# Optimization experiments

Measured on AMD Instinct MI355X. Metric: run time of the kernel, lower is better.

The kernel has to match this reference:

```python
import jax, jax.numpy as jnp
import numpy as np

B, C, S, H, W, J = 4, 256, 256, 128, 128, 8
BN_EPS = 1e-5


def _conv3x3(x, w, b):
    # x: [B,S,H,W], w: [C,S,3,3] (OIHW), SAME padding, stride 1
    y = jax.lax.conv_general_dilated(x, w, window_strides=(1, 1), padding='SAME',
                                     dimension_numbers=('NCHW', 'OIHW', 'NCHW'))
    return y + b[None, :, None, None]


def setup_inputs() -> dict:
    key = jax.random.key(0)
    ks = jax.random.split(key, 12)
    fp = jax.random.normal(ks[0], (B, C, H, W), jnp.float32)
    labels = jax.random.randint(ks[1], (B, H, W), 0, J)
    sg = jax.nn.one_hot(labels, J, axis=1, dtype=jnp.float32)  # [B,J,H,W], disjoint masks
    style_codes = jax.random.normal(ks[2], (B, J + 1, S), jnp.float32)
    mask_codes = jax.random.randint(ks[3], (B, J), 0, 2)  # 0 or 1
    bn_gamma = 1.0 + 0.1 * jax.random.normal(ks[4], (C,), jnp.float32)
    bn_beta = 0.1 * jax.random.normal(ks[5], (C,), jnp.float32)
    W_mu = 0.05 * jax.random.normal(ks[6], (J, S, S), jnp.float32)
    b_mu = 0.05 * jax.random.normal(ks[7], (J, S), jnp.float32)
    W_gamma = 0.05 * jax.random.normal(ks[8], (C, S, 3, 3), jnp.float32)
    b_gamma = 0.05 * jax.random.normal(ks[9], (C,), jnp.float32)
    W_beta = 0.05 * jax.random.normal(ks[10], (C, S, 3, 3), jnp.float32)
    b_beta = 0.05 * jax.random.normal(ks[11], (C,), jnp.float32)
    return {"fp": fp, "sg": sg, "style_codes": style_codes, "mask_codes": mask_codes,
            "bn_gamma": bn_gamma, "bn_beta": bn_beta, "W_mu": W_mu, "b_mu": b_mu,
            "W_gamma": W_gamma, "b_gamma": b_gamma, "W_beta": W_beta, "b_beta": b_beta}


def reference(fp, sg, style_codes, mask_codes, bn_gamma, bn_beta,
              W_mu, b_mu, W_gamma, b_gamma, W_beta, b_beta):
    # BatchNorm2d (training mode, biased variance, affine)
    mean = jnp.mean(fp, axis=(0, 2, 3))
    var = jnp.mean(jnp.square(fp - mean[None, :, None, None]), axis=(0, 2, 3))
    nf = (fp - mean[None, :, None, None]) * jax.lax.rsqrt(var + BN_EPS)[None, :, None, None]
    nf = nf * bn_gamma[None, :, None, None] + bn_beta[None, :, None, None]

    # per-(batch,class) style code selection: j if mask_codes==1 else J (shared code)
    sel = jnp.where(mask_codes == 1, jnp.arange(J, dtype=mask_codes.dtype)[None, :], J)  # [B,J]
    codes = jnp.take_along_axis(style_codes, sel[:, :, None], axis=1)  # [B,J,S]

    # per-class FC + ReLU (torch Linear: y = x @ W.T + b)
    mu = jax.nn.relu(jnp.einsum('bjs,jos->bjo', codes, W_mu) + b_mu[None])  # [B,J,S]

    # scatter per-region style into spatial map (masks are disjoint one-hot)
    middle = jnp.einsum('bjhw,bjs->bshw', sg, mu)  # [B,S,H,W]

    gamma_avg = _conv3x3(middle, W_gamma, b_gamma)
    beta_avg = _conv3x3(middle, W_beta, b_beta)
    return nf * (1.0 + gamma_avg) + beta_avg
```

## Files before the change

### kernel.cpp

```cpp
#include <hip/hip_runtime.h>

#define Bb 4
#define Cc 256
#define Ss 256
#define Hh 128
#define Ww 128
#define Jj 8
#define HWp 16384
#define BN_EPS 1e-5f

#define WS_PS   0
#define WS_PQ   4096
#define WS_MU   10240
#define WS_LAB  43008
#define WS_WTG  108544
#define WS_WTB  2467840
#define WS_VT   4827136

#define VROW 160
#define ZOFF (81 * VROW)
#define SLICE (2 * ZOFF)
#define VBUF_B 26112

__global__ void k_prep(const float* __restrict__ fp, const float* __restrict__ sg,
                       const float* __restrict__ style, const int* __restrict__ mask,
                       const float* __restrict__ Wmu, const float* __restrict__ bmu,
                       const float* __restrict__ Wg, const float* __restrict__ Wb,
                       float* __restrict__ ws_f, unsigned char* __restrict__ labout,
                       float* __restrict__ muout,
                       float* __restrict__ wtg, float* __restrict__ wtb) {
    __shared__ float smem[1056];
    const int t = threadIdx.x;
    const int blk = blockIdx.x;
    if (blk < 1024) {
        const int c = blk >> 2, b = blk & 3;
        const float4* s4 = (const float4*)(fp + (size_t)(b * Cc + c) * HWp);
        float sum = 0.f, sq = 0.f;
        #pragma unroll
        for (int k = 0; k < 16; ++k) {
            float4 v = s4[t + k * 256];
            sum += v.x + v.y + v.z + v.w;
            sq  += v.x * v.x + v.y * v.y + v.z * v.z + v.w * v.w;
        }
        float* ls = smem;
        float* lq = smem + 256;
        ls[t] = sum; lq[t] = sq;
        __syncthreads();
        for (int off = 128; off > 0; off >>= 1) {
            if (t < off) { ls[t] += ls[t + off]; lq[t] += lq[t + off]; }
            __syncthreads();
        }
        if (t == 0) { ws_f[blk] = ls[0]; ws_f[1024 + blk] = lq[0]; }
    } else if (blk < 1280) {
        const int i = (blk - 1024) * 256 + t;
        const int b = i >> 14, p = i & (HWp - 1);
        const float* base = sg + (size_t)b * Jj * HWp + p;
        int l = 0;
        #pragma unroll
        for (int j = 0; j < Jj; ++j)
            if (base[(size_t)j * HWp] > 0.5f) l = j;
        labout[i] = (unsigned char)l;
    } else if (blk < 1312) {
        const int lb = blk - 1280;
        const int b = lb >> 3, j = lb & 7;
        const int sel = (mask[b * Jj + j] == 1) ? j : Jj;
        float* code = smem;
        code[t] = style[(size_t)(b * (Jj + 1) + sel) * Ss + t];
        __syncthreads();
        const float4* wrow = (const float4*)(Wmu + (size_t)(j * Ss + t) * Ss);
        const float4* c4 = (const float4*)code;
        float acc = bmu[j * Ss + t];
        #pragma unroll 8
        for (int s4i = 0; s4i < Ss / 4; ++s4i) {
            float4 w = wrow[s4i]; float4 cv = c4[s4i];
            acc += w.x * cv.x + w.y * cv.y + w.z * cv.z + w.w * cv.w;
        }
        muout[(size_t)lb * Ss + t] = fmaxf(acc, 0.f);
    } else {
        const int local = blk - 1312;
        const int z = local / 576;
        const int rem = local % 576;
        const int k0 = (rem % 72) * 32;
        const int r0 = (rem / 72) * 32;
        const float* in = z ? Wb : Wg;
        float* outp = z ? wtb : wtg;
        float (*tile)[33] = (float(*)[33])smem;
        const int tx = t & 31, ty = t >> 5;
        #pragma unroll
        for (int i2 = 0; i2 < 4; ++i2)
            tile[ty + 8 * i2][tx] = in[(size_t)(r0 + ty + 8 * i2) * 2304 + k0 + tx];
        __syncthreads();
        #pragma unroll
        for (int i2 = 0; i2 < 4; ++i2)
            outp[(size_t)(k0 + ty + 8 * i2) * 256 + r0 + tx] = tile[tx][ty + 8 * i2];
    }
}

__global__ void k_build(const float* __restrict__ bn_g, const float* __restrict__ bn_b,
                        const float* __restrict__ bgam, const float* __restrict__ bbet,
                        const float* __restrict__ wtg, const float* __restrict__ wtb,
                        const float* __restrict__ mu, float* __restrict__ ws_f,
                        float* __restrict__ vt) {
    const int t = threadIdx.x;
    if (blockIdx.x == 0) {
        float s = 0.f, q = 0.f;
        #pragma unroll
        for (int b = 0; b < 4; ++b) { s += ws_f[t * 4 + b]; q += ws_f[1024 + t * 4 + b]; }
        float mean = s * (1.f / 65536.f);
        float var  = q * (1.f / 65536.f) - mean * mean;
        float sc = bn_g[t] * rsqrtf(var + BN_EPS);
        float sh = bn_b[t] - mean * sc;
        ((float4*)ws_f)[t] = make_float4(sc, sh, 1.f + bgam[t], bbet[t]);
        return;
    }
    const int lb = blockIdx.x - 1;
    const int z = lb / 36;
    const int rem = lb % 36;
    const int tap = rem % 9, b = rem / 9;
    const float* Wt = z ? wtb : wtg;
    __shared__ __align__(16) float ml[Jj * Ss];
    for (int idx = t; idx < Jj * Ss; idx += 256)
        ml[idx] = mu[(size_t)b * Jj * Ss + (size_t)(idx & 7) * Ss + (idx >> 3)];
    __syncthreads();
    float ag[8] = {0,0,0,0,0,0,0,0};
    const float* wp = Wt + (size_t)tap * 256 + t;
    #pragma unroll 8
    for (int s = 0; s < Ss; ++s) {
        float wv = wp[(size_t)s * 2304];
        float4 m0 = *(const float4*)&ml[s * 8];
        float4 m1 = *(const float4*)&ml[s * 8 + 4];
        ag[0] += wv * m0.x; ag[1] += wv * m0.y;
        ag[2] += wv * m0.z; ag[3] += wv * m0.w;
        ag[4] += wv * m1.x; ag[5] += wv * m1.y;
        ag[6] += wv * m1.z; ag[7] += wv * m1.w;
    }
    const int cc = t >> 5, cl = t & 31;
    float* Vrow = vt + ((size_t)((cc * 4 + b) * 2 + z) * 81 + tap * 9) * 40 + cl;
    #pragma unroll
    for (int j = 0; j < 8; ++j) Vrow[j * 40] = ag[j];
    Vrow[8 * 40] = 0.f;
}

__global__ void __launch_bounds__(256, 4) k_main(
    const float* __restrict__ fp, const unsigned char* __restrict__ lab,
    const char* __restrict__ vt, const float4* __restrict__ T,
    float* __restrict__ out) {
    const int h0 = blockIdx.x * 4, cc = blockIdx.y, b = blockIdx.z;
    __shared__ __align__(16) char vbuf[VBUF_B];
    __shared__ int labs[6][132];
    __shared__ float4 Tl[32];
    const int t = threadIdx.x;
    const int lane = t & 63;
    const int wid = __builtin_amdgcn_readfirstlane(t >> 6);

    {
        const char* slice = vt + (size_t)(cc * 4 + b) * SLICE;
        for (int r = wid; r < 102; r += 4) {
            __builtin_amdgcn_global_load_lds(
                (const __attribute__((address_space(1))) void*)(slice + r * 256 + lane * 4),
                (__attribute__((address_space(3))) void*)(vbuf + r * 256), 4, 0, 0);
        }
    }
    if (t < 32) Tl[t] = T[cc * 32 + t];
    for (int idx = t; idx < 6 * 132; idx += 256) {
        const int r = idx / 132, col = idx % 132 - 1;
        const int hh = h0 - 1 + r;
        int v = 8;
        if (hh >= 0 && hh < Hh && col >= 0 && col < Ww)
            v = lab[((size_t)b << 14) + (hh << 7) + col];
        labs[r][idx % 132] = v;
    }
    __syncthreads();

    const int w = t & 127;
    const int cs = t >> 7;
    const int cbase = cc * 32 + cs * 16;

    for (int hh = 0; hh < 4; ++hh) {
        int vb0[9];
        #pragma unroll
        for (int tap = 0; tap < 9; ++tap) {
            const int j = labs[hh + tap / 3][w + tap % 3];
            vb0[tap] = (tap * 9 + j) * VROW + cs * 64;
        }
        const size_t io = ((size_t)(b * Cc + cbase) << 14) + ((h0 + hh) << 7) + w;
        const float* fpp = fp + io;
        float* outp = out + io;
        #pragma unroll
        for (int cb = 0; cb < 4; ++cb) {
            float4 ga = make_float4(0.f, 0.f, 0.f, 0.f);
            float4 ea = make_float4(0.f, 0.f, 0.f, 0.f);
            #pragma unroll
            for (int tap = 0; tap < 9; ++tap) {
                const float4 vg = *(const float4*)(vbuf + vb0[tap] + cb * 16);
                const float4 ve = *(const float4*)(vbuf + ZOFF + vb0[tap] + cb * 16);
                ga.x += vg.x; ga.y += vg.y; ga.z += vg.z; ga.w += vg.w;
                ea.x += ve.x; ea.y += ve.y; ea.z += ve.z; ea.w += ve.w;
            }
            #define APPLY(CI, GV, EV)                                              \
            {                                                                      \
                const int c = cb * 4 + CI;                                         \
                const float4 tv = Tl[cs * 16 + c];                                 \
                const float f = __builtin_nontemporal_load(fpp + (size_t)c * HWp); \
                const float nf = fmaf(f, tv.x, tv.y);                              \
                __builtin_nontemporal_store(fmaf(nf, tv.z + (GV), tv.w + (EV)),    \
                                            outp + (size_t)c * HWp);               \
            }
            APPLY(0, ga.x, ea.x)
            APPLY(1, ga.y, ea.y)
            APPLY(2, ga.z, ea.z)
            APPLY(3, ga.w, ea.w)
            #undef APPLY
        }
    }
}

extern "C" void kernel_launch(void* const* d_in, const int* in_sizes, int n_in,
                              void* d_out, int out_size, void* d_ws, size_t ws_size,
                              hipStream_t stream) {
    const float* fp      = (const float*)d_in[0];
    const float* sg      = (const float*)d_in[1];
    const float* style   = (const float*)d_in[2];
    const int*   mask    = (const int*)d_in[3];
    const float* bn_g    = (const float*)d_in[4];
    const float* bn_b    = (const float*)d_in[5];
    const float* W_mu    = (const float*)d_in[6];
    const float* b_mu    = (const float*)d_in[7];
    const float* W_gam   = (const float*)d_in[8];
    const float* b_gam   = (const float*)d_in[9];
    const float* W_bet   = (const float*)d_in[10];
    const float* b_bet   = (const float*)d_in[11];
    float* out = (float*)d_out;

    char* ws = (char*)d_ws;
    float*         ws_f  = (float*)ws;
    unsigned char* labp  = (unsigned char*)(ws + WS_LAB);
    float*         mup   = (float*)(ws + WS_MU);
    float*         wtg   = (float*)(ws + WS_WTG);
    float*         wtb   = (float*)(ws + WS_WTB);
    float*         vtp   = (float*)(ws + WS_VT);

    k_prep<<<2464, 256, 0, stream>>>(fp, sg, style, mask, W_mu, b_mu, W_gam, W_bet,
                                     ws_f, labp, mup, wtg, wtb);
    k_build<<<73, 256, 0, stream>>>(bn_g, bn_b, b_gam, b_bet, wtg, wtb, mup, ws_f, vtp);
    k_main<<<dim3(32, 8, 4), 256, 0, stream>>>(fp, labp, (const char*)vtp,
                                               (const float4*)ws_f, out);
}
```

Baseline: 71.57 us.

## Halve channels per main block, shrink LDS table, split build over class halves

The main kernel now covers 16 channels per block instead of 32, which halves its shared-memory table and doubles the grid. It raises the occupancy hint to 8 blocks per CU and stages the table with 16-byte global-to-LDS loads. The build kernel splits its work over two class halves to match the new per-slice layout and to launch more blocks. The trade-off is that label-tile loads and setup are repeated across twice as many blocks.

```diff
diff --git a/kernel.cpp b/kernel.cpp
--- a/kernel.cpp
+++ b/kernel.cpp
@@ -17,10 +17,10 @@
 #define WS_WTB  2467840
 #define WS_VT   4827136
 
-#define VROW 160
-#define ZOFF (81 * VROW)
-#define SLICE (2 * ZOFF)
-#define VBUF_B 26112
+#define VROW 80
+#define ZOFF 6480
+#define SLICE_B 13312
+#define SLICE_F 3328
 
 __global__ void k_prep(const float* __restrict__ fp, const float* __restrict__ sg,
                        const float* __restrict__ style, const int* __restrict__ mask,
@@ -114,54 +114,54 @@
         return;
     }
     const int lb = blockIdx.x - 1;
-    const int z = lb / 36;
-    const int rem = lb % 36;
-    const int tap = rem % 9, b = rem / 9;
+    const int z = lb / 72;
+    const int rem = lb % 72;
+    const int jh = rem / 36;
+    const int r2 = rem % 36;
+    const int tap = r2 % 9, b = r2 / 9;
     const float* Wt = z ? wtb : wtg;
-    __shared__ __align__(16) float ml[Jj * Ss];
-    for (int idx = t; idx < Jj * Ss; idx += 256)
-        ml[idx] = mu[(size_t)b * Jj * Ss + (size_t)(idx & 7) * Ss + (idx >> 3)];
+    __shared__ __align__(16) float ml[4 * Ss];
+    for (int idx = t; idx < 4 * Ss; idx += 256)
+        ml[idx] = mu[(size_t)b * Jj * Ss + (size_t)(jh * 4 + (idx & 3)) * Ss + (idx >> 2)];
     __syncthreads();
-    float ag[8] = {0,0,0,0,0,0,0,0};
+    float ag[4] = {0, 0, 0, 0};
     const float* wp = Wt + (size_t)tap * 256 + t;
     #pragma unroll 8
     for (int s = 0; s < Ss; ++s) {
         float wv = wp[(size_t)s * 2304];
-        float4 m0 = *(const float4*)&ml[s * 8];
-        float4 m1 = *(const float4*)&ml[s * 8 + 4];
-        ag[0] += wv * m0.x; ag[1] += wv * m0.y;
-        ag[2] += wv * m0.z; ag[3] += wv * m0.w;
-        ag[4] += wv * m1.x; ag[5] += wv * m1.y;
-        ag[6] += wv * m1.z; ag[7] += wv * m1.w;
-    }
-    const int cc = t >> 5, cl = t & 31;
-    float* Vrow = vt + ((size_t)((cc * 4 + b) * 2 + z) * 81 + tap * 9) * 40 + cl;
+        float4 m = *(const float4*)&ml[s * 4];
+        ag[0] += wv * m.x; ag[1] += wv * m.y;
+        ag[2] += wv * m.z; ag[3] += wv * m.w;
+    }
+    const int cc = t >> 4, cl = t & 15;
+    float* Vrow = vt + (size_t)(cc * 4 + b) * SLICE_F + z * 1620
+                + (tap * 9 + jh * 4) * 20 + cl;
     #pragma unroll
-    for (int j = 0; j < 8; ++j) Vrow[j * 40] = ag[j];
-    Vrow[8 * 40] = 0.f;
-}
-
-__global__ void __launch_bounds__(256, 4) k_main(
+    for (int jj = 0; jj < 4; ++jj) Vrow[jj * 20] = ag[jj];
+    if (jh == 1) Vrow[4 * 20] = 0.f;
+}
+
+__global__ void __launch_bounds__(256, 8) k_main(
     const float* __restrict__ fp, const unsigned char* __restrict__ lab,
     const char* __restrict__ vt, const float4* __restrict__ T,
     float* __restrict__ out) {
     const int h0 = blockIdx.x * 4, cc = blockIdx.y, b = blockIdx.z;
-    __shared__ __align__(16) char vbuf[VBUF_B];
+    __shared__ __align__(16) char vbuf[SLICE_B];
     __shared__ int labs[6][132];
-    __shared__ float4 Tl[32];
+    __shared__ float4 Tl[16];
     const int t = threadIdx.x;
     const int lane = t & 63;
     const int wid = __builtin_amdgcn_readfirstlane(t >> 6);
 
     {
-        const char* slice = vt + (size_t)(cc * 4 + b) * SLICE;
-        for (int r = wid; r < 102; r += 4) {
+        const char* slice = vt + (size_t)(cc * 4 + b) * SLICE_B;
+        for (int r = wid; r < 13; r += 4) {
             __builtin_amdgcn_global_load_lds(
-                (const __attribute__((address_space(1))) void*)(slice + r * 256 + lane * 4),
-                (__attribute__((address_space(3))) void*)(vbuf + r * 256), 4, 0, 0);
-        }
-    }
-    if (t < 32) Tl[t] = T[cc * 32 + t];
+                (const __attribute__((address_space(1))) void*)(slice + r * 1024 + lane * 16),
+                (__attribute__((address_space(3))) void*)(vbuf + r * 1024), 16, 0, 0);
+        }
+    }
+    if (t < 16) Tl[t] = T[cc * 16 + t];
     for (int idx = t; idx < 6 * 132; idx += 256) {
         const int r = idx / 132, col = idx % 132 - 1;
         const int hh = h0 - 1 + r;
@@ -174,20 +174,20 @@
 
     const int w = t & 127;
     const int cs = t >> 7;
-    const int cbase = cc * 32 + cs * 16;
+    const int cbase = cc * 16 + cs * 8;
 
     for (int hh = 0; hh < 4; ++hh) {
         int vb0[9];
         #pragma unroll
         for (int tap = 0; tap < 9; ++tap) {
             const int j = labs[hh + tap / 3][w + tap % 3];
-            vb0[tap] = (tap * 9 + j) * VROW + cs * 64;
+            vb0[tap] = (tap * 9 + j) * VROW + cs * 32;
         }
         const size_t io = ((size_t)(b * Cc + cbase) << 14) + ((h0 + hh) << 7) + w;
         const float* fpp = fp + io;
         float* outp = out + io;
         #pragma unroll
-        for (int cb = 0; cb < 4; ++cb) {
+        for (int cb = 0; cb < 2; ++cb) {
             float4 ga = make_float4(0.f, 0.f, 0.f, 0.f);
             float4 ea = make_float4(0.f, 0.f, 0.f, 0.f);
             #pragma unroll
@@ -200,7 +200,7 @@
             #define APPLY(CI, GV, EV)                                              \
             {                                                                      \
                 const int c = cb * 4 + CI;                                         \
-                const float4 tv = Tl[cs * 16 + c];                                 \
+                const float4 tv = Tl[cs * 8 + c];                                  \
                 const float f = __builtin_nontemporal_load(fpp + (size_t)c * HWp); \
                 const float nf = fmaf(f, tv.x, tv.y);                              \
                 __builtin_nontemporal_store(fmaf(nf, tv.z + (GV), tv.w + (EV)),    \
@@ -242,7 +242,7 @@
 
     k_prep<<<2464, 256, 0, stream>>>(fp, sg, style, mask, W_mu, b_mu, W_gam, W_bet,
                                      ws_f, labp, mup, wtg, wtb);
-    k_build<<<73, 256, 0, stream>>>(bn_g, bn_b, b_gam, b_bet, wtg, wtb, mup, ws_f, vtp);
-    k_main<<<dim3(32, 8, 4), 256, 0, stream>>>(fp, labp, (const char*)vtp,
-                                               (const float4*)ws_f, out);
-}
+    k_build<<<145, 256, 0, stream>>>(bn_g, bn_b, b_gam, b_bet, wtg, wtb, mup, ws_f, vtp);
+    k_main<<<dim3(32, 16, 4), 256, 0, stream>>>(fp, labp, (const char*)vtp,
+                                                (const float4*)ws_f, out);
+}
```

New measurement: 75.16 us. 5.0% more time.

## Interleave gamma/beta V table rows, halve rows per block, batch LDS loads

Applied to the files above, without the earlier changes.

The precomputed per-(tap,label) gamma and beta contributions are now stored interleaved in one 272-byte row instead of two separate planes. This shrinks each slice so it can be staged into LDS with 16-byte global_load_lds transfers. Each k_main block now handles 2 output rows instead of 4, so the grid doubles and launch bounds allow 8 blocks per CU, aiming at more occupancy and better latency hiding. The 9-tap reductions are split into grouped LDS loads with sched barriers and tree-shaped sums, trading more VGPRs and more repeated slice loads per output for higher memory-level parallelism.

```diff
diff --git a/kernel.cpp b/kernel.cpp
--- a/kernel.cpp
+++ b/kernel.cpp
@@ -17,10 +17,9 @@
 #define WS_WTB  2467840
 #define WS_VT   4827136
 
-#define VROW 160
-#define ZOFF (81 * VROW)
-#define SLICE (2 * ZOFF)
-#define VBUF_B 26112
+#define VROW 272
+#define SLICE_B 22528
+#define SLICE_F 5632
 
 __global__ void k_prep(const float* __restrict__ fp, const float* __restrict__ sg,
                        const float* __restrict__ style, const int* __restrict__ mask,
@@ -135,34 +134,34 @@
         ag[6] += wv * m1.z; ag[7] += wv * m1.w;
     }
     const int cc = t >> 5, cl = t & 31;
-    float* Vrow = vt + ((size_t)((cc * 4 + b) * 2 + z) * 81 + tap * 9) * 40 + cl;
+    float* base = vt + (size_t)(cc * 4 + b) * SLICE_F + z * 32 + cl;
     #pragma unroll
-    for (int j = 0; j < 8; ++j) Vrow[j * 40] = ag[j];
-    Vrow[8 * 40] = 0.f;
-}
-
-__global__ void __launch_bounds__(256, 4) k_main(
+    for (int j = 0; j < 8; ++j) base[(tap * 9 + j) * 68] = ag[j];
+    base[(tap * 9 + 8) * 68] = 0.f;
+}
+
+__global__ void __launch_bounds__(256, 8) k_main(
     const float* __restrict__ fp, const unsigned char* __restrict__ lab,
     const char* __restrict__ vt, const float4* __restrict__ T,
     float* __restrict__ out) {
-    const int h0 = blockIdx.x * 4, cc = blockIdx.y, b = blockIdx.z;
-    __shared__ __align__(16) char vbuf[VBUF_B];
-    __shared__ int labs[6][132];
+    const int h0 = blockIdx.x * 2, cc = blockIdx.y, b = blockIdx.z;
+    __shared__ __align__(16) char vbuf[SLICE_B];
+    __shared__ int labs[4][132];
     __shared__ float4 Tl[32];
     const int t = threadIdx.x;
     const int lane = t & 63;
     const int wid = __builtin_amdgcn_readfirstlane(t >> 6);
 
     {
-        const char* slice = vt + (size_t)(cc * 4 + b) * SLICE;
-        for (int r = wid; r < 102; r += 4) {
+        const char* slice = vt + (size_t)(cc * 4 + b) * SLICE_B;
+        for (int r = wid; r < 22; r += 4) {
             __builtin_amdgcn_global_load_lds(
-                (const __attribute__((address_space(1))) void*)(slice + r * 256 + lane * 4),
-                (__attribute__((address_space(3))) void*)(vbuf + r * 256), 4, 0, 0);
+                (const __attribute__((address_space(1))) void*)(slice + r * 1024 + lane * 16),
+                (__attribute__((address_space(3))) void*)(vbuf + r * 1024), 16, 0, 0);
         }
     }
     if (t < 32) Tl[t] = T[cc * 32 + t];
-    for (int idx = t; idx < 6 * 132; idx += 256) {
+    for (int idx = t; idx < 4 * 132; idx += 256) {
         const int r = idx / 132, col = idx % 132 - 1;
         const int hh = h0 - 1 + r;
         int v = 8;
@@ -176,7 +175,7 @@
     const int cs = t >> 7;
     const int cbase = cc * 32 + cs * 16;
 
-    for (int hh = 0; hh < 4; ++hh) {
+    for (int hh = 0; hh < 2; ++hh) {
         int vb0[9];
         #pragma unroll
         for (int tap = 0; tap < 9; ++tap) {
@@ -188,15 +187,34 @@
         float* outp = out + io;
         #pragma unroll
         for (int cb = 0; cb < 4; ++cb) {
-            float4 ga = make_float4(0.f, 0.f, 0.f, 0.f);
-            float4 ea = make_float4(0.f, 0.f, 0.f, 0.f);
+            float4 vg[9];
             #pragma unroll
-            for (int tap = 0; tap < 9; ++tap) {
-                const float4 vg = *(const float4*)(vbuf + vb0[tap] + cb * 16);
-                const float4 ve = *(const float4*)(vbuf + ZOFF + vb0[tap] + cb * 16);
-                ga.x += vg.x; ga.y += vg.y; ga.z += vg.z; ga.w += vg.w;
-                ea.x += ve.x; ea.y += ve.y; ea.z += ve.z; ea.w += ve.w;
-            }
+            for (int tap = 0; tap < 9; ++tap)
+                vg[tap] = *(const float4*)(vbuf + vb0[tap] + cb * 16);
+            __builtin_amdgcn_sched_barrier(0);
+            float4 ve[9];
+            #pragma unroll
+            for (int tap = 0; tap < 9; ++tap)
+                ve[tap] = *(const float4*)(vbuf + vb0[tap] + 128 + cb * 16);
+            float4 ga;
+            ga.x = ((vg[0].x + vg[1].x) + (vg[2].x + vg[3].x)) +
+                   ((vg[4].x + vg[5].x) + (vg[6].x + vg[7].x)) + vg[8].x;
+            ga.y = ((vg[0].y + vg[1].y) + (vg[2].y + vg[3].y)) +
+                   ((vg[4].y + vg[5].y) + (vg[6].y + vg[7].y)) + vg[8].y;
+            ga.z = ((vg[0].z + vg[1].z) + (vg[2].z + vg[3].z)) +
+                   ((vg[4].z + vg[5].z) + (vg[6].z + vg[7].z)) + vg[8].z;
+            ga.w = ((vg[0].w + vg[1].w) + (vg[2].w + vg[3].w)) +
+                   ((vg[4].w + vg[5].w) + (vg[6].w + vg[7].w)) + vg[8].w;
+            __builtin_amdgcn_sched_barrier(0);
+            float4 ea;
+            ea.x = ((ve[0].x + ve[1].x) + (ve[2].x + ve[3].x)) +
+                   ((ve[4].x + ve[5].x) + (ve[6].x + ve[7].x)) + ve[8].x;
+            ea.y = ((ve[0].y + ve[1].y) + (ve[2].y + ve[3].y)) +
+                   ((ve[4].y + ve[5].y) + (ve[6].y + ve[7].y)) + ve[8].y;
+            ea.z = ((ve[0].z + ve[1].z) + (ve[2].z + ve[3].z)) +
+                   ((ve[4].z + ve[5].z) + (ve[6].z + ve[7].z)) + ve[8].z;
+            ea.w = ((ve[0].w + ve[1].w) + (ve[2].w + ve[3].w)) +
+                   ((ve[4].w + ve[5].w) + (ve[6].w + ve[7].w)) + ve[8].w;
             #define APPLY(CI, GV, EV)                                              \
             {                                                                      \
                 const int c = cb * 4 + CI;                                         \
@@ -243,6 +261,6 @@
     k_prep<<<2464, 256, 0, stream>>>(fp, sg, style, mask, W_mu, b_mu, W_gam, W_bet,
                                      ws_f, labp, mup, wtg, wtb);
     k_build<<<73, 256, 0, stream>>>(bn_g, bn_b, b_gam, b_bet, wtg, wtb, mup, ws_f, vtp);
-    k_main<<<dim3(32, 8, 4), 256, 0, stream>>>(fp, labp, (const char*)vtp,
+    k_main<<<dim3(64, 8, 4), 256, 0, stream>>>(fp, labp, (const char*)vtp,
                                                (const float4*)ws_f, out);
 }
```

After: 68.77 us. 1.04x faster.
